# Kernel tuning notes

Measured on AMD Instinct MI355X. Metric: run time of the kernel, lower is better.

Reference implementation:

```python
import jax, jax.numpy as jnp
import numpy as np

H = 4          # number of GCN heads (hard-coded self.h = 4)
EPS = 1e-6     # MWPToolkit LayerNorm eps
B, K, D, HID = 16, 1024, 256, 256
DK = D // H


def setup_inputs() -> dict:
    key = jax.random.key(0)
    ks = jax.random.split(key, 12)
    sc = lambda fan_in: 1.0 / np.sqrt(fan_in).astype(np.float32)
    return {
        "graph_nodes": jax.random.normal(ks[0], (B, K, D), jnp.float32),
        "graph": jax.random.randint(ks[1], (B, 5, K, K), 0, 2, jnp.int32),
        # per-head GCN layer 1: GraphConvolution(indim -> hiddim)
        "Wg1": jax.random.normal(ks[2], (H, D, HID), jnp.float32) * sc(D),
        "bg1": jax.random.normal(ks[3], (H, HID), jnp.float32) * sc(D),
        # per-head GCN layer 2: GraphConvolution(hiddim -> d_k)
        "Wg2": jax.random.normal(ks[4], (H, HID, DK), jnp.float32) * sc(HID),
        "bg2": jax.random.normal(ks[5], (H, DK), jnp.float32) * sc(HID),
        # PositionwiseFeedForward: Linear(indim,hiddim) -> ReLU -> Linear(hiddim,outdim)
        "Wf1": jax.random.normal(ks[6], (D, HID), jnp.float32) * sc(D),
        "bf1": jax.random.normal(ks[7], (HID,), jnp.float32) * sc(D),
        "Wf2": jax.random.normal(ks[8], (HID, D), jnp.float32) * sc(HID),
        "bf2": jax.random.normal(ks[9], (D,), jnp.float32) * sc(HID),
        # LayerNorm(outdim) affine params
        "ln_a": jnp.ones((D,), jnp.float32),
        "ln_b": jnp.zeros((D,), jnp.float32),
    }


def reference(graph_nodes, graph, Wg1, bg1, Wg2, bg2, Wf1, bf1, Wf2, bf2, ln_a, ln_b):
    adj = graph.astype(jnp.float32)                      # (B, 5, K, K)
    # adj_list = [adj[:,1], adj[:,1], adj[:,4], adj[:,4]] -> stack heads
    adj_h = jnp.stack([adj[:, 1], adj[:, 1], adj[:, 4], adj[:, 4]])  # (H,B,K,K)

    # GCN layer 1 (all heads at once): relu(adj @ (x @ W1) + b1)
    sup1 = jnp.einsum('bkd,hdf->hbkf', graph_nodes, Wg1)            # (H,B,K,HID)
    h1 = jax.nn.relu(jnp.einsum('hbkj,hbjf->hbkf', adj_h, sup1)
                     + bg1[:, None, None, :])
    # (dropout is identity in eval)
    # GCN layer 2: adj @ (h1 @ W2) + b2
    sup2 = jnp.einsum('hbkf,hfe->hbke', h1, Wg2)                    # (H,B,K,DK)
    h2 = jnp.einsum('hbkj,hbje->hbke', adj_h, sup2) + bg2[:, None, None, :]

    # concat heads along feature dim: (B,K,H*DK) == (B,K,D)
    g = jnp.transpose(h2, (1, 2, 0, 3)).reshape(h2.shape[1], h2.shape[2], -1)

    # MWPToolkit LayerNorm: a*(x-mean)/(std+eps)+b, std unbiased (ddof=1)
    mu = g.mean(-1, keepdims=True)
    sd = jnp.std(g, axis=-1, keepdims=True, ddof=1)
    g = ln_a * (g - mu) / (sd + EPS) + ln_b + graph_nodes           # residual

    # PositionwiseFeedForward + residual (dropout identity in eval)
    ff = jax.nn.relu(g @ Wf1 + bf1) @ Wf2 + bf2
    out = ff + g
    return adj, out
```

## Files before the change

### kernel.cpp

```cpp
#include <hip/hip_runtime.h>

typedef unsigned short ushort_t;
using short8  = __attribute__((ext_vector_type(8))) short;
using floatx4 = __attribute__((ext_vector_type(4))) float;

__device__ __forceinline__ ushort_t f2bf(float f) {
  unsigned int x = __builtin_bit_cast(unsigned int, f);
  x += 0x7fffu + ((x >> 16) & 1u);
  return (ushort_t)(x >> 16);
}

__device__ __forceinline__ float bf2f(ushort_t h) {
  return __builtin_bit_cast(float, (unsigned int)h << 16);
}

__device__ __forceinline__ void gld16(const ushort_t* g, ushort_t* l) {
  __builtin_amdgcn_global_load_lds(
      (const __attribute__((address_space(1))) void*)(unsigned long long)(uintptr_t)g,
      (__attribute__((address_space(3))) void*)l, 16, 0, 0);
}

template <typename F>
__device__ __forceinline__ void gemm_tile(const ushort_t* __restrict__ A, int lda,
                                          const ushort_t* __restrict__ BT, int ldb,
                                          int K, F epi) {
  __shared__ ushort_t As[128 * 64];
  __shared__ ushort_t Bs[128 * 64];

  const int tid  = threadIdx.x;
  const int wave = tid >> 6;
  const int lane = tid & 63;
  const int l15  = lane & 15;
  const int quad = lane >> 4;
  const int wm   = wave >> 1;
  const int wn   = wave & 1;

  const int srow8  = lane >> 3;
  const int schunk = lane & 7;
  const int gcol   = ((schunk ^ srow8) * 8);

  const ushort_t* gA = A  + (size_t)(wave * 32 + srow8) * lda + gcol;
  const ushort_t* gB = BT + (size_t)(wave * 32 + srow8) * ldb + gcol;
  ushort_t* lA = As + (wave * 32) * 64;
  ushort_t* lB = Bs + (wave * 32) * 64;

  floatx4 acc[4][4] = {};
  const int arow0 = (wm * 64 + l15) * 64;
  const int brow0 = (wn * 64 + l15) * 64;
  const int cx    = l15 & 7;

  for (int k0 = 0; k0 < K; k0 += 64) {
#pragma unroll
    for (int ci = 0; ci < 4; ci++) {
      gld16(gA + (size_t)(ci * 8) * lda, lA + ci * 512);
      gld16(gB + (size_t)(ci * 8) * ldb, lB + ci * 512);
    }
    gA += 64; gB += 64;
    __syncthreads();
#pragma unroll
    for (int ks = 0; ks < 2; ks++) {
      const int cs = ((ks * 4 + quad) ^ cx) * 8;
      short8 af[4], bfr[4];
#pragma unroll
      for (int i = 0; i < 4; i++) af[i]  = *(const short8*)(As + arow0 + i * 1024 + cs);
#pragma unroll
      for (int j = 0; j < 4; j++) bfr[j] = *(const short8*)(Bs + brow0 + j * 1024 + cs);
#pragma unroll
      for (int i = 0; i < 4; i++)
#pragma unroll
        for (int j = 0; j < 4; j++)
          acc[i][j] = __builtin_amdgcn_mfma_f32_16x16x32_bf16(af[i], bfr[j], acc[i][j], 0, 0, 0);
    }
    __syncthreads();
  }

#pragma unroll
  for (int i = 0; i < 4; i++)
#pragma unroll
    for (int j = 0; j < 4; j++)
#pragma unroll
      for (int r = 0; r < 4; r++)
        epi(wm * 64 + i * 16 + quad * 4 + r, wn * 64 + j * 16 + l15, acc[i][j][r]);
}

template <typename F>
__device__ __forceinline__ void gemm_tile64(const ushort_t* __restrict__ A, int lda,
                                            const ushort_t* __restrict__ BT, int ldb,
                                            int K, F epi) {
  __shared__ ushort_t As[64 * 64];
  __shared__ ushort_t Bs[128 * 64];

  const int tid  = threadIdx.x;
  const int wave = tid >> 6;
  const int lane = tid & 63;
  const int l15  = lane & 15;
  const int quad = lane >> 4;
  const int wm   = wave >> 1;
  const int wn   = wave & 1;

  const int srow8  = lane >> 3;
  const int schunk = lane & 7;
  const int gcol   = ((schunk ^ srow8) * 8);

  const ushort_t* gA = A  + (size_t)(wave * 16 + srow8) * lda + gcol;
  const ushort_t* gB = BT + (size_t)(wave * 32 + srow8) * ldb + gcol;
  ushort_t* lA = As + (wave * 16) * 64;
  ushort_t* lB = Bs + (wave * 32) * 64;

  floatx4 acc[2][4] = {};
  const int arow0 = (wm * 32 + l15) * 64;
  const int brow0 = (wn * 64 + l15) * 64;
  const int cx    = l15 & 7;

  for (int k0 = 0; k0 < K; k0 += 64) {
#pragma unroll
    for (int ci = 0; ci < 2; ci++)
      gld16(gA + (size_t)(ci * 8) * lda, lA + ci * 512);
#pragma unroll
    for (int ci = 0; ci < 4; ci++)
      gld16(gB + (size_t)(ci * 8) * ldb, lB + ci * 512);
    gA += 64; gB += 64;
    __syncthreads();
#pragma unroll
    for (int ks = 0; ks < 2; ks++) {
      const int cs = ((ks * 4 + quad) ^ cx) * 8;
      short8 af[2], bfr[4];
#pragma unroll
      for (int i = 0; i < 2; i++) af[i]  = *(const short8*)(As + arow0 + i * 1024 + cs);
#pragma unroll
      for (int j = 0; j < 4; j++) bfr[j] = *(const short8*)(Bs + brow0 + j * 1024 + cs);
#pragma unroll
      for (int i = 0; i < 2; i++)
#pragma unroll
        for (int j = 0; j < 4; j++)
          acc[i][j] = __builtin_amdgcn_mfma_f32_16x16x32_bf16(af[i], bfr[j], acc[i][j], 0, 0, 0);
    }
    __syncthreads();
  }

#pragma unroll
  for (int i = 0; i < 2; i++)
#pragma unroll
    for (int j = 0; j < 4; j++)
#pragma unroll
      for (int r = 0; r < 4; r++)
        epi(wm * 32 + i * 16 + quad * 4 + r, wn * 64 + j * 16 + l15, acc[i][j][r]);
}


__global__ __launch_bounds__(256) void k_cast(const int* __restrict__ graph,
                                              float* __restrict__ adj_out,
                                              ushort_t* __restrict__ adjb) {
  const size_t i = (size_t)blockIdx.x * 256 + threadIdx.x;
  int4 v = ((const int4*)graph)[i];
  float4 f = make_float4((float)v.x, (float)v.y, (float)v.z, (float)v.w);
  ((float4*)adj_out)[i] = f;
  const size_t e0 = i * 4;
  const unsigned sb = (unsigned)(e0 >> 20);
  const unsigned s = sb % 5u, b = sb / 5u;
  if (s == 1u || s == 4u) {
    const unsigned tt = (s == 4u) ? 1u : 0u;
    ushort4 h;
    h.x = f2bf(f.x); h.y = f2bf(f.y); h.z = f2bf(f.z); h.w = f2bf(f.w);
    *(ushort4*)(adjb + (((size_t)(b * 2 + tt)) << 20) + (e0 & 0xFFFFFu)) = h;
  }
}

__global__ __launch_bounds__(256) void k_xt(const float* __restrict__ gn,
                                            ushort_t* __restrict__ XT) {
  __shared__ float t[64][68];
  const int b = blockIdx.z, dt = blockIdx.y, kt = blockIdx.x;
  const int r  = threadIdx.x >> 4;
  const int c4 = (threadIdx.x & 15) * 4;
#pragma unroll
  for (int rr = 0; rr < 4; rr++) {
    const int kl = rr * 16 + r;
    float4 v = *(const float4*)(gn + ((size_t)(b * 1024 + kt * 64 + kl)) * 256 + dt * 64 + c4);
    t[kl][c4] = v.x; t[kl][c4 + 1] = v.y; t[kl][c4 + 2] = v.z; t[kl][c4 + 3] = v.w;
  }
  __syncthreads();
#pragma unroll
  for (int rr = 0; rr < 4; rr++) {
    const int dl = rr * 16 + r;
    ushort4 h;
    h.x = f2bf(t[c4][dl]);     h.y = f2bf(t[c4 + 1][dl]);
    h.z = f2bf(t[c4 + 2][dl]); h.w = f2bf(t[c4 + 3][dl]);
    *(ushort4*)(XT + ((size_t)(b * 256 + dt * 64 + dl)) * 1024 + kt * 64 + c4) = h;
  }
}

__global__ __launch_bounds__(256) void k_prepw(const float* __restrict__ Wg1, const float* __restrict__ Wg2,
                                               const float* __restrict__ Wf1, const float* __restrict__ Wf2,
                                               ushort_t* __restrict__ W1T, ushort_t* __restrict__ W2pT,
                                               ushort_t* __restrict__ Wf1T, ushort_t* __restrict__ Wf2T) {
  const int i = blockIdx.x * 256 + threadIdx.x;
  if (i < 262144) {
    const int fI = i >> 8, d = i & 255;
    const int h = fI >> 8, ff = fI & 255;
    W1T[i] = f2bf(Wg1[((h << 8) + d) * 256 + ff]);
  } else if (i < 393216) {
    const int j = i - 262144;
    const int t = j >> 16, rem = j & 65535;
    const int ep = rem >> 9, k = rem & 511;
    const int hh = ep >> 6;
    const float v = ((k >> 8) == hh)
        ? Wg2[(((t * 2 + hh) << 8) + (k & 255)) * 64 + (ep & 63)] : 0.f;
    W2pT[j] = f2bf(v);
  } else if (i < 458752) {
    const int j = i - 393216;
    const int n = j >> 8, k = j & 255;
    Wf1T[j] = f2bf(Wf1[k * 256 + n]);
  } else if (i < 524288) {
    const int j = i - 458752;
    const int n = j >> 8, k = j & 255;
    Wf2T[j] = f2bf(Wf2[k * 256 + n]);
  }
}


__global__ __launch_bounds__(256) void k_ax(const ushort_t* __restrict__ adjb,
                                            const ushort_t* __restrict__ XT,
                                            ushort_t* __restrict__ AX) {
  const int nt = blockIdx.x, mt = blockIdx.y, bt = blockIdx.z;
  const int b = bt >> 1;
  const ushort_t* A  = adjb + ((size_t)bt << 20) + (size_t)mt * 128 * 1024;
  const ushort_t* BT = XT + ((size_t)b << 18) + (size_t)nt * 128 * 1024;
  ushort_t* C = AX + ((size_t)bt << 18);
  gemm_tile(A, 1024, BT, 1024, 1024, [&](int r, int c, float v) {
    C[(size_t)(mt * 128 + r) * 256 + nt * 128 + c] = f2bf(v);
  });
}

__global__ __launch_bounds__(256) void k_h1(const ushort_t* __restrict__ AX,
                                            const ushort_t* __restrict__ W1T,
                                            const float* __restrict__ bg1,
                                            ushort_t* __restrict__ h1) {
  const int nt = blockIdx.x, mt = blockIdx.y, b = blockIdx.z;
  const int t = nt >> 2;
  const ushort_t* A  = AX + ((size_t)(b * 2 + t) << 18) + (size_t)mt * 128 * 256;
  const ushort_t* BT = W1T + (size_t)nt * 128 * 256;
  ushort_t* C = h1 + ((size_t)b << 20);
  const float* bias = bg1 + nt * 128;
  gemm_tile(A, 256, BT, 256, 256, [&](int r, int c, float v) {
    C[(size_t)(mt * 128 + r) * 1024 + nt * 128 + c] = f2bf(fmaxf(v + bias[c], 0.f));
  });
}

__global__ __launch_bounds__(256) void k_g3(const ushort_t* __restrict__ W2pT,
                                            const ushort_t* __restrict__ h1,
                                            ushort_t* __restrict__ sup2T) {
  const int mx = blockIdx.x, nt = blockIdx.y, bt = blockIdx.z;
  const int b = bt >> 1, t = bt & 1;
  const ushort_t* A  = W2pT + (size_t)t * 65536 + (size_t)mx * 64 * 512;
  const ushort_t* BT = h1 + ((size_t)b << 20) + (size_t)nt * 131072 + t * 512;
  ushort_t* C = sup2T + (size_t)bt * 131072;
  gemm_tile64(A, 512, BT, 1024, 512, [&](int r, int c, float v) {
    C[(size_t)(mx * 64 + r) * 1024 + nt * 128 + c] = f2bf(v);
  });
}

__global__ __launch_bounds__(256) void k_g4ln(const ushort_t* __restrict__ adjb,
                                              const ushort_t* __restrict__ sup2T,
                                              const float* __restrict__ bg2,
                                              const float* __restrict__ gn,
                                              const float* __restrict__ la,
                                              const float* __restrict__ lb,
                                              ushort_t* __restrict__ glnb) {
  __shared__ ushort_t As[64 * 64];
  __shared__ ushort_t Bs[256 * 64];
  __shared__ float sred[4][32], qred[4][32];

  const int mt = blockIdx.x, b = blockIdx.y;
  const int tid = threadIdx.x, wave = tid >> 6, lane = tid & 63;
  const int l15 = lane & 15, quad = lane >> 4;
  const int wn = wave;
  const int tsel = wn >> 1;

  const int srow8 = lane >> 3, schunk = lane & 7;
  const int gcol = (schunk ^ srow8) * 8;

  const ushort_t* gA = adjb + ((size_t)(b * 2 + (wave >> 1)) << 20)
                     + (size_t)(mt * 32 + (wave & 1) * 16 + srow8) * 1024 + gcol;
  const ushort_t* gB = sup2T + (size_t)(b * 2 + (wave >> 1)) * 131072
                     + (size_t)((wave & 1) * 64 + srow8) * 1024 + gcol;
  ushort_t* lA = As + (wave * 16) * 64;
  ushort_t* lB = Bs + (wave * 64) * 64;

  floatx4 acc[2][4] = {};
  const int arow0 = (tsel * 32 + l15) * 64;
  const int brow0 = (wn * 64 + l15) * 64;
  const int cx = l15 & 7;

  for (int k0 = 0; k0 < 1024; k0 += 64) {
#pragma unroll
    for (int ci = 0; ci < 2; ci++)
      gld16(gA + (size_t)(ci * 8) * 1024, lA + ci * 512);
#pragma unroll
    for (int ci = 0; ci < 8; ci++)
      gld16(gB + (size_t)(ci * 8) * 1024, lB + ci * 512);
    gA += 64; gB += 64;
    __syncthreads();
#pragma unroll
    for (int ks = 0; ks < 2; ks++) {
      const int cs = ((ks * 4 + quad) ^ cx) * 8;
      short8 af[2], bfr[4];
#pragma unroll
      for (int i = 0; i < 2; i++) af[i]  = *(const short8*)(As + arow0 + i * 1024 + cs);
#pragma unroll
      for (int j = 0; j < 4; j++) bfr[j] = *(const short8*)(Bs + brow0 + j * 1024 + cs);
#pragma unroll
      for (int i = 0; i < 2; i++)
#pragma unroll
        for (int j = 0; j < 4; j++)
          acc[i][j] = __builtin_amdgcn_mfma_f32_16x16x32_bf16(af[i], bfr[j], acc[i][j], 0, 0, 0);
    }
    __syncthreads();
  }

  float laj[4], lbj[4];
#pragma unroll
  for (int j = 0; j < 4; j++) {
    const int colg = wn * 64 + j * 16 + l15;
    const float bj = bg2[colg];
    laj[j] = la[colg]; lbj[j] = lb[colg];
#pragma unroll
    for (int i = 0; i < 2; i++)
#pragma unroll
      for (int r = 0; r < 4; r++) acc[i][j][r] += bj;
  }

#pragma unroll
  for (int i = 0; i < 2; i++)
#pragma unroll
    for (int r = 0; r < 4; r++) {
      float s = 0.f, q = 0.f;
#pragma unroll
      for (int j = 0; j < 4; j++) { const float v = acc[i][j][r]; s += v; q += v * v; }
#pragma unroll
      for (int m = 1; m < 16; m <<= 1) { s += __shfl_xor(s, m); q += __shfl_xor(q, m); }
      if (l15 == 0) {
        const int row = i * 16 + quad * 4 + r;
        sred[wn][row] = s; qred[wn][row] = q;
      }
    }
  __syncthreads();

  const size_t rowbase = (size_t)(b * 1024 + mt * 32);
#pragma unroll
  for (int i = 0; i < 2; i++)
#pragma unroll
    for (int r = 0; r < 4; r++) {
      const int row = i * 16 + quad * 4 + r;
      const float S = sred[0][row] + sred[1][row] + sred[2][row] + sred[3][row];
      const float Q = qred[0][row] + qred[1][row] + qred[2][row] + qred[3][row];
      const float mu = S * (1.f / 256.f);
      const float var = fmaxf((Q - S * mu) * (1.f / 255.f), 0.f);
      const float inv = 1.f / (sqrtf(var) + 1e-6f);
      const float* gnr = gn + (rowbase + row) * 256;
      ushort_t* outr = glnb + (rowbase + row) * 256;
#pragma unroll
      for (int j = 0; j < 4; j++) {
        const int colg = wn * 64 + j * 16 + l15;
        const float o = laj[j] * (acc[i][j][r] - mu) * inv + lbj[j] + gnr[colg];
        outr[colg] = f2bf(o);
      }
    }
}

__global__ __launch_bounds__(256) void k_f1(const ushort_t* __restrict__ gln,
                                            const ushort_t* __restrict__ Wf1T,
                                            const float* __restrict__ bf1,
                                            ushort_t* __restrict__ tb) {
  const int nt = blockIdx.x, mt = blockIdx.y;
  const ushort_t* A  = gln + (size_t)mt * 64 * 256;
  const ushort_t* BT = Wf1T + (size_t)nt * 128 * 256;
  const float* bias = bf1 + nt * 128;
  gemm_tile64(A, 256, BT, 256, 256, [&](int r, int c, float v) {
    tb[(size_t)(mt * 64 + r) * 256 + nt * 128 + c] = f2bf(fmaxf(v + bias[c], 0.f));
  });
}

__global__ __launch_bounds__(256) void k_f2(const ushort_t* __restrict__ tb,
                                            const ushort_t* __restrict__ Wf2T,
                                            const float* __restrict__ bf2,
                                            const ushort_t* __restrict__ glnb,
                                            float* __restrict__ out) {
  const int nt = blockIdx.x, mt = blockIdx.y;
  const ushort_t* A  = tb + (size_t)mt * 64 * 256;
  const ushort_t* BT = Wf2T + (size_t)nt * 128 * 256;
  const float* bias = bf2 + nt * 128;
  gemm_tile64(A, 256, BT, 256, 256, [&](int r, int c, float v) {
    const size_t idx = (size_t)(mt * 64 + r) * 256 + nt * 128 + c;
    out[idx] = v + bias[c] + bf2f(glnb[idx]);
  });
}

extern "C" void kernel_launch(void* const* d_in, const int* in_sizes, int n_in,
                              void* d_out, int out_size, void* d_ws, size_t ws_size,
                              hipStream_t stream) {
  const float* gnodes = (const float*)d_in[0];
  const int*   graph  = (const int*)d_in[1];
  const float* Wg1 = (const float*)d_in[2];
  const float* bg1 = (const float*)d_in[3];
  const float* Wg2 = (const float*)d_in[4];
  const float* bg2 = (const float*)d_in[5];
  const float* Wf1 = (const float*)d_in[6];
  const float* bf1 = (const float*)d_in[7];
  const float* Wf2 = (const float*)d_in[8];
  const float* bf2 = (const float*)d_in[9];
  const float* ln_a = (const float*)d_in[10];
  const float* ln_b = (const float*)d_in[11];

  float* adj_out = (float*)d_out;
  float* out     = (float*)d_out + 83886080;

  char* ws = (char*)d_ws;
  ushort_t* adjb  = (ushort_t*)(ws);
  ushort_t* XT    = (ushort_t*)(ws + 67108864);
  ushort_t* W1T   = (ushort_t*)(ws + 75497472);
  ushort_t* W2pT  = (ushort_t*)(ws + 76021760);
  ushort_t* Wf1T  = (ushort_t*)(ws + 76283904);
  ushort_t* Wf2T  = (ushort_t*)(ws + 76414976);
  ushort_t* AX    = (ushort_t*)(ws + 76546048);
  ushort_t* h1    = (ushort_t*)(ws + 93323264);
  ushort_t* sup2T = (ushort_t*)(ws + 126877696);
  ushort_t* glnb  = (ushort_t*)(ws + 135266304);
  ushort_t* tbuf  = (ushort_t*)(ws + 143654912);

  k_xt   <<<dim3(16, 4, 16), 256, 0, stream>>>(gnodes, XT);
  k_prepw<<<2048, 256, 0, stream>>>(Wg1, Wg2, Wf1, Wf2, W1T, W2pT, Wf1T, Wf2T);
  k_cast <<<81920, 256, 0, stream>>>(graph, adj_out, adjb);

  k_ax<<<dim3(2, 8, 32), 256, 0, stream>>>(adjb, XT, AX);
  k_h1<<<dim3(8, 8, 16), 256, 0, stream>>>(AX, W1T, bg1, h1);
  k_g3<<<dim3(2, 8, 32), 256, 0, stream>>>(W2pT, h1, sup2T);
  k_g4ln<<<dim3(32, 16), 256, 0, stream>>>(adjb, sup2T, bg2, gnodes, ln_a, ln_b, glnb);

  k_f1<<<dim3(2, 256), 256, 0, stream>>>(glnb, Wf1T, bf1, tbuf);
  k_f2<<<dim3(2, 256), 256, 0, stream>>>(tbuf, Wf2T, bf2, glnb, out);
}
```

Measured before the change: 693.4 us.

## Fuse prep kernels into one launch and fold FFN GEMMs into LayerNorm tail

Merges the three preprocessing kernels (adjacency cast, node transpose, weight prep) into a single launch that dispatches on block index. Fuses the two feed-forward GEMMs and the residual into the GCN-layer-2/LayerNorm kernel. The normalized tile and the ReLU intermediate stay in shared memory, and the residual is kept in registers. This removes the glnb and tbuf round-trips through global memory and two launches, at the cost of more shared memory per block and only 512 blocks doing the FFN work.

```diff
diff --git a/kernel.cpp b/kernel.cpp
--- a/kernel.cpp
+++ b/kernel.cpp
@@ -8,10 +8,6 @@
   unsigned int x = __builtin_bit_cast(unsigned int, f);
   x += 0x7fffu + ((x >> 16) & 1u);
   return (ushort_t)(x >> 16);
-}
-
-__device__ __forceinline__ float bf2f(ushort_t h) {
-  return __builtin_bit_cast(float, (unsigned int)h << 16);
 }
 
 __device__ __forceinline__ void gld16(const ushort_t* g, ushort_t* l) {
@@ -147,73 +143,74 @@
         epi(wm * 32 + i * 16 + quad * 4 + r, wn * 64 + j * 16 + l15, acc[i][j][r]);
 }
 
-
-__global__ __launch_bounds__(256) void k_cast(const int* __restrict__ graph,
+__global__ __launch_bounds__(256) void k_prep(const int* __restrict__ graph,
                                               float* __restrict__ adj_out,
-                                              ushort_t* __restrict__ adjb) {
-  const size_t i = (size_t)blockIdx.x * 256 + threadIdx.x;
-  int4 v = ((const int4*)graph)[i];
-  float4 f = make_float4((float)v.x, (float)v.y, (float)v.z, (float)v.w);
-  ((float4*)adj_out)[i] = f;
-  const size_t e0 = i * 4;
-  const unsigned sb = (unsigned)(e0 >> 20);
-  const unsigned s = sb % 5u, b = sb / 5u;
-  if (s == 1u || s == 4u) {
-    const unsigned tt = (s == 4u) ? 1u : 0u;
-    ushort4 h;
-    h.x = f2bf(f.x); h.y = f2bf(f.y); h.z = f2bf(f.z); h.w = f2bf(f.w);
-    *(ushort4*)(adjb + (((size_t)(b * 2 + tt)) << 20) + (e0 & 0xFFFFFu)) = h;
-  }
-}
-
-__global__ __launch_bounds__(256) void k_xt(const float* __restrict__ gn,
-                                            ushort_t* __restrict__ XT) {
+                                              ushort_t* __restrict__ adjb,
+                                              const float* __restrict__ gn,
+                                              ushort_t* __restrict__ XT,
+                                              const float* __restrict__ Wg1, const float* __restrict__ Wg2,
+                                              const float* __restrict__ Wf1, const float* __restrict__ Wf2,
+                                              ushort_t* __restrict__ W1T, ushort_t* __restrict__ W2pT,
+                                              ushort_t* __restrict__ Wf1T, ushort_t* __restrict__ Wf2T) {
   __shared__ float t[64][68];
-  const int b = blockIdx.z, dt = blockIdx.y, kt = blockIdx.x;
-  const int r  = threadIdx.x >> 4;
-  const int c4 = (threadIdx.x & 15) * 4;
-#pragma unroll
-  for (int rr = 0; rr < 4; rr++) {
-    const int kl = rr * 16 + r;
-    float4 v = *(const float4*)(gn + ((size_t)(b * 1024 + kt * 64 + kl)) * 256 + dt * 64 + c4);
-    t[kl][c4] = v.x; t[kl][c4 + 1] = v.y; t[kl][c4 + 2] = v.z; t[kl][c4 + 3] = v.w;
-  }
-  __syncthreads();
-#pragma unroll
-  for (int rr = 0; rr < 4; rr++) {
-    const int dl = rr * 16 + r;
-    ushort4 h;
-    h.x = f2bf(t[c4][dl]);     h.y = f2bf(t[c4 + 1][dl]);
-    h.z = f2bf(t[c4 + 2][dl]); h.w = f2bf(t[c4 + 3][dl]);
-    *(ushort4*)(XT + ((size_t)(b * 256 + dt * 64 + dl)) * 1024 + kt * 64 + c4) = h;
-  }
-}
-
-__global__ __launch_bounds__(256) void k_prepw(const float* __restrict__ Wg1, const float* __restrict__ Wg2,
-                                               const float* __restrict__ Wf1, const float* __restrict__ Wf2,
-                                               ushort_t* __restrict__ W1T, ushort_t* __restrict__ W2pT,
-                                               ushort_t* __restrict__ Wf1T, ushort_t* __restrict__ Wf2T) {
-  const int i = blockIdx.x * 256 + threadIdx.x;
-  if (i < 262144) {
-    const int fI = i >> 8, d = i & 255;
-    const int h = fI >> 8, ff = fI & 255;
-    W1T[i] = f2bf(Wg1[((h << 8) + d) * 256 + ff]);
-  } else if (i < 393216) {
-    const int j = i - 262144;
-    const int t = j >> 16, rem = j & 65535;
-    const int ep = rem >> 9, k = rem & 511;
-    const int hh = ep >> 6;
-    const float v = ((k >> 8) == hh)
-        ? Wg2[(((t * 2 + hh) << 8) + (k & 255)) * 64 + (ep & 63)] : 0.f;
-    W2pT[j] = f2bf(v);
-  } else if (i < 458752) {
-    const int j = i - 393216;
-    const int n = j >> 8, k = j & 255;
-    Wf1T[j] = f2bf(Wf1[k * 256 + n]);
-  } else if (i < 524288) {
-    const int j = i - 458752;
-    const int n = j >> 8, k = j & 255;
-    Wf2T[j] = f2bf(Wf2[k * 256 + n]);
+  const int bid = blockIdx.x;
+  if (bid < 81920) {
+    const size_t i = (size_t)bid * 256 + threadIdx.x;
+    int4 v = ((const int4*)graph)[i];
+    float4 f = make_float4((float)v.x, (float)v.y, (float)v.z, (float)v.w);
+    ((float4*)adj_out)[i] = f;
+    const size_t e0 = i * 4;
+    const unsigned sb = (unsigned)(e0 >> 20);
+    const unsigned s = sb % 5u, b = sb / 5u;
+    if (s == 1u || s == 4u) {
+      const unsigned tt = (s == 4u) ? 1u : 0u;
+      ushort4 h;
+      h.x = f2bf(f.x); h.y = f2bf(f.y); h.z = f2bf(f.z); h.w = f2bf(f.w);
+      *(ushort4*)(adjb + (((size_t)(b * 2 + tt)) << 20) + (e0 & 0xFFFFFu)) = h;
+    }
+  } else if (bid < 82944) {
+    const int id = bid - 81920;
+    const int kt = id & 15, dt = (id >> 4) & 3, b = id >> 6;
+    const int r  = threadIdx.x >> 4;
+    const int c4 = (threadIdx.x & 15) * 4;
+#pragma unroll
+    for (int rr = 0; rr < 4; rr++) {
+      const int kl = rr * 16 + r;
+      float4 v = *(const float4*)(gn + ((size_t)(b * 1024 + kt * 64 + kl)) * 256 + dt * 64 + c4);
+      t[kl][c4] = v.x; t[kl][c4 + 1] = v.y; t[kl][c4 + 2] = v.z; t[kl][c4 + 3] = v.w;
+    }
+    __syncthreads();
+#pragma unroll
+    for (int rr = 0; rr < 4; rr++) {
+      const int dl = rr * 16 + r;
+      ushort4 h;
+      h.x = f2bf(t[c4][dl]);     h.y = f2bf(t[c4 + 1][dl]);
+      h.z = f2bf(t[c4 + 2][dl]); h.w = f2bf(t[c4 + 3][dl]);
+      *(ushort4*)(XT + ((size_t)(b * 256 + dt * 64 + dl)) * 1024 + kt * 64 + c4) = h;
+    }
+  } else {
+    const int i = (bid - 82944) * 256 + threadIdx.x;
+    if (i < 262144) {
+      const int fI = i >> 8, d = i & 255;
+      const int h = fI >> 8, ff = fI & 255;
+      W1T[i] = f2bf(Wg1[((h << 8) + d) * 256 + ff]);
+    } else if (i < 393216) {
+      const int j = i - 262144;
+      const int tt = j >> 16, rem = j & 65535;
+      const int ep = rem >> 9, k = rem & 511;
+      const int hh = ep >> 6;
+      const float v = ((k >> 8) == hh)
+          ? Wg2[(((tt * 2 + hh) << 8) + (k & 255)) * 64 + (ep & 63)] : 0.f;
+      W2pT[j] = f2bf(v);
+    } else if (i < 458752) {
+      const int j = i - 393216;
+      const int n = j >> 8, k = j & 255;
+      Wf1T[j] = f2bf(Wf1[k * 256 + n]);
+    } else if (i < 524288) {
+      const int j = i - 458752;
+      const int n = j >> 8, k = j & 255;
+      Wf2T[j] = f2bf(Wf2[k * 256 + n]);
+    }
   }
 }
 
@@ -259,15 +256,21 @@
   });
 }
 
-__global__ __launch_bounds__(256) void k_g4ln(const ushort_t* __restrict__ adjb,
+__global__ __launch_bounds__(256) void k_tail(const ushort_t* __restrict__ adjb,
                                               const ushort_t* __restrict__ sup2T,
                                               const float* __restrict__ bg2,
                                               const float* __restrict__ gn,
                                               const float* __restrict__ la,
                                               const float* __restrict__ lb,
-                                              ushort_t* __restrict__ glnb) {
+                                              const ushort_t* __restrict__ Wf1T,
+                                              const float* __restrict__ bf1,
+                                              const ushort_t* __restrict__ Wf2T,
+                                              const float* __restrict__ bf2,
+                                              float* __restrict__ out) {
   __shared__ ushort_t As[64 * 64];
   __shared__ ushort_t Bs[256 * 64];
+  __shared__ ushort_t Ps[32 * 256];
+  __shared__ ushort_t Ts[32 * 256];
   __shared__ float sred[4][32], qred[4][32];
 
   const int mt = blockIdx.x, b = blockIdx.y;
@@ -328,7 +331,6 @@
 #pragma unroll
       for (int r = 0; r < 4; r++) acc[i][j][r] += bj;
   }
-
 #pragma unroll
   for (int i = 0; i < 2; i++)
 #pragma unroll
@@ -346,6 +348,7 @@
   __syncthreads();
 
   const size_t rowbase = (size_t)(b * 1024 + mt * 32);
+  float glnreg[2][4][4];
 #pragma unroll
   for (int i = 0; i < 2; i++)
 #pragma unroll
@@ -357,42 +360,99 @@
       const float var = fmaxf((Q - S * mu) * (1.f / 255.f), 0.f);
       const float inv = 1.f / (sqrtf(var) + 1e-6f);
       const float* gnr = gn + (rowbase + row) * 256;
-      ushort_t* outr = glnb + (rowbase + row) * 256;
 #pragma unroll
       for (int j = 0; j < 4; j++) {
         const int colg = wn * 64 + j * 16 + l15;
-        const float o = laj[j] * (acc[i][j][r] - mu) * inv + lbj[j] + gnr[colg];
-        outr[colg] = f2bf(o);
-      }
-    }
-}
-
-__global__ __launch_bounds__(256) void k_f1(const ushort_t* __restrict__ gln,
-                                            const ushort_t* __restrict__ Wf1T,
-                                            const float* __restrict__ bf1,
-                                            ushort_t* __restrict__ tb) {
-  const int nt = blockIdx.x, mt = blockIdx.y;
-  const ushort_t* A  = gln + (size_t)mt * 64 * 256;
-  const ushort_t* BT = Wf1T + (size_t)nt * 128 * 256;
-  const float* bias = bf1 + nt * 128;
-  gemm_tile64(A, 256, BT, 256, 256, [&](int r, int c, float v) {
-    tb[(size_t)(mt * 64 + r) * 256 + nt * 128 + c] = f2bf(fmaxf(v + bias[c], 0.f));
-  });
-}
-
-__global__ __launch_bounds__(256) void k_f2(const ushort_t* __restrict__ tb,
-                                            const ushort_t* __restrict__ Wf2T,
-                                            const float* __restrict__ bf2,
-                                            const ushort_t* __restrict__ glnb,
-                                            float* __restrict__ out) {
-  const int nt = blockIdx.x, mt = blockIdx.y;
-  const ushort_t* A  = tb + (size_t)mt * 64 * 256;
-  const ushort_t* BT = Wf2T + (size_t)nt * 128 * 256;
-  const float* bias = bf2 + nt * 128;
-  gemm_tile64(A, 256, BT, 256, 256, [&](int r, int c, float v) {
-    const size_t idx = (size_t)(mt * 64 + r) * 256 + nt * 128 + c;
-    out[idx] = v + bias[c] + bf2f(glnb[idx]);
-  });
+        const float g = laj[j] * (acc[i][j][r] - mu) * inv + lbj[j] + gnr[colg];
+        glnreg[i][j][r] = g;
+        Ps[row * 256 + ((((colg >> 3) ^ row) & 31) << 3) + (colg & 7)] = f2bf(g);
+      }
+    }
+  __syncthreads();
+
+  floatx4 acc2[2][4] = {};
+  for (int k0 = 0; k0 < 256; k0 += 64) {
+#pragma unroll
+    for (int ci = 0; ci < 8; ci++)
+      gld16(Wf1T + (size_t)(wave * 64 + ci * 8 + srow8) * 256 + k0 + gcol,
+            Bs + (wave * 64 + ci * 8) * 64);
+    __syncthreads();
+#pragma unroll
+    for (int ks = 0; ks < 2; ks++) {
+      const int c32 = (k0 >> 3) + ks * 4 + quad;
+      const int cs = ((ks * 4 + quad) ^ cx) * 8;
+      short8 af[2], bfr[4];
+#pragma unroll
+      for (int i = 0; i < 2; i++) {
+        const int row = i * 16 + l15;
+        af[i] = *(const short8*)(Ps + row * 256 + (((c32 ^ row) & 31) << 3));
+      }
+#pragma unroll
+      for (int j = 0; j < 4; j++) bfr[j] = *(const short8*)(Bs + brow0 + j * 1024 + cs);
+#pragma unroll
+      for (int i = 0; i < 2; i++)
+#pragma unroll
+        for (int j = 0; j < 4; j++)
+          acc2[i][j] = __builtin_amdgcn_mfma_f32_16x16x32_bf16(af[i], bfr[j], acc2[i][j], 0, 0, 0);
+    }
+    __syncthreads();
+  }
+
+#pragma unroll
+  for (int j = 0; j < 4; j++) {
+    const int colg = wn * 64 + j * 16 + l15;
+    const float bj = bf1[colg];
+#pragma unroll
+    for (int i = 0; i < 2; i++)
+#pragma unroll
+      for (int r = 0; r < 4; r++) {
+        const int row = i * 16 + quad * 4 + r;
+        const float v = fmaxf(acc2[i][j][r] + bj, 0.f);
+        Ts[row * 256 + ((((colg >> 3) ^ row) & 31) << 3) + (colg & 7)] = f2bf(v);
+      }
+  }
+  __syncthreads();
+
+  floatx4 acc3[2][4] = {};
+  for (int k0 = 0; k0 < 256; k0 += 64) {
+#pragma unroll
+    for (int ci = 0; ci < 8; ci++)
+      gld16(Wf2T + (size_t)(wave * 64 + ci * 8 + srow8) * 256 + k0 + gcol,
+            Bs + (wave * 64 + ci * 8) * 64);
+    __syncthreads();
+#pragma unroll
+    for (int ks = 0; ks < 2; ks++) {
+      const int c32 = (k0 >> 3) + ks * 4 + quad;
+      const int cs = ((ks * 4 + quad) ^ cx) * 8;
+      short8 af[2], bfr[4];
+#pragma unroll
+      for (int i = 0; i < 2; i++) {
+        const int row = i * 16 + l15;
+        af[i] = *(const short8*)(Ts + row * 256 + (((c32 ^ row) & 31) << 3));
+      }
+#pragma unroll
+      for (int j = 0; j < 4; j++) bfr[j] = *(const short8*)(Bs + brow0 + j * 1024 + cs);
+#pragma unroll
+      for (int i = 0; i < 2; i++)
+#pragma unroll
+        for (int j = 0; j < 4; j++)
+          acc3[i][j] = __builtin_amdgcn_mfma_f32_16x16x32_bf16(af[i], bfr[j], acc3[i][j], 0, 0, 0);
+    }
+    __syncthreads();
+  }
+
+#pragma unroll
+  for (int j = 0; j < 4; j++) {
+    const int colg = wn * 64 + j * 16 + l15;
+    const float bj = bf2[colg];
+#pragma unroll
+    for (int i = 0; i < 2; i++)
+#pragma unroll
+      for (int r = 0; r < 4; r++) {
+        const int row = i * 16 + quad * 4 + r;
+        out[(rowbase + row) * 256 + colg] = acc3[i][j][r] + bj + glnreg[i][j][r];
+      }
+  }
 }
 
 extern "C" void kernel_launch(void* const* d_in, const int* in_sizes, int n_in,
@@ -424,18 +484,13 @@
   ushort_t* AX    = (ushort_t*)(ws + 76546048);
   ushort_t* h1    = (ushort_t*)(ws + 93323264);
   ushort_t* sup2T = (ushort_t*)(ws + 126877696);
-  ushort_t* glnb  = (ushort_t*)(ws + 135266304);
-  ushort_t* tbuf  = (ushort_t*)(ws + 143654912);
-
-  k_xt   <<<dim3(16, 4, 16), 256, 0, stream>>>(gnodes, XT);
-  k_prepw<<<2048, 256, 0, stream>>>(Wg1, Wg2, Wf1, Wf2, W1T, W2pT, Wf1T, Wf2T);
-  k_cast <<<81920, 256, 0, stream>>>(graph, adj_out, adjb);
+
+  k_prep<<<84992, 256, 0, stream>>>(graph, adj_out, adjb, gnodes, XT,
+                                    Wg1, Wg2, Wf1, Wf2, W1T, W2pT, Wf1T, Wf2T);
 
   k_ax<<<dim3(2, 8, 32), 256, 0, stream>>>(adjb, XT, AX);
   k_h1<<<dim3(8, 8, 16), 256, 0, stream>>>(AX, W1T, bg1, h1);
   k_g3<<<dim3(2, 8, 32), 256, 0, stream>>>(W2pT, h1, sup2T);
-  k_g4ln<<<dim3(32, 16), 256, 0, stream>>>(adjb, sup2T, bg2, gnodes, ln_a, ln_b, glnb);
-
-  k_f1<<<dim3(2, 256), 256, 0, stream>>>(glnb, Wf1T, bf1, tbuf);
-  k_f2<<<dim3(2, 256), 256, 0, stream>>>(tbuf, Wf2T, bf2, glnb, out);
-}
+  k_tail<<<dim3(32, 16), 256, 0, stream>>>(adjb, sup2T, bg2, gnodes, ln_a, ln_b,
+                                           Wf1T, bf1, Wf2T, bf2, out);
+}
```

After: 665.0 us. 1.04x faster.
